# Optimization experiments

Measured on AMD Instinct MI355X. Metric: run time of the kernel, lower is better.

The kernel has to match this reference:

```python
import jax, jax.numpy as jnp
import numpy as np

N, C, H, W = 16, 80, 200, 152
STRIDE = 8
PRE_NMS_THRESH = 0.2
K = 100            # pre_nms_top_n (== fpn_post_nms_top_n)
NMS_THRESH = 0.6
MIN_SIZE = 0.0


def setup_inputs() -> dict:
    key = jax.random.key(0)
    k1, k2, k3 = jax.random.split(key, 3)
    # shift logits down so only a realistic fraction passes sigmoid > 0.2
    box_cls = jax.random.normal(k1, (N, C, H, W), jnp.float32) - 2.0
    box_regression = jax.random.uniform(k2, (N, 4, H, W), jnp.float32) * 64.0
    centerness = jax.random.normal(k3, (N, 1, H, W), jnp.float32)
    ys, xs = jnp.meshgrid(jnp.arange(H), jnp.arange(W), indexing='ij')
    locations = jnp.stack([xs * STRIDE + STRIDE // 2,
                           ys * STRIDE + STRIDE // 2], axis=-1)
    locations = locations.reshape(-1, 2).astype(jnp.float32)  # [HW, 2] (x, y)
    return {"locations": locations, "box_cls": box_cls,
            "box_regression": box_regression, "centerness": centerness,
            "size_h": H * STRIDE, "size_w": W * STRIDE}


def _iou_matrix(boxes):
    # boxes: [K, 4] xyxy -> pairwise IoU [K, K]
    area = jnp.clip(boxes[:, 2] - boxes[:, 0], 0) * jnp.clip(boxes[:, 3] - boxes[:, 1], 0)
    lt = jnp.maximum(boxes[:, None, :2], boxes[None, :, :2])
    rb = jnp.minimum(boxes[:, None, 2:], boxes[None, :, 2:])
    wh = jnp.clip(rb - lt, 0)
    inter = wh[..., 0] * wh[..., 1]
    return inter / (area[:, None] + area[None, :] - inter + 1e-9)


def _nms_keep(iou, valid):
    # boxes assumed sorted by score (desc). Sequential greedy suppression.
    k = valid.shape[0]
    ar = jnp.arange(k)
    def body(i, keep):
        suppressed = jnp.any(keep & (ar < i) & (iou[i] > NMS_THRESH))
        return keep.at[i].set(valid[i] & ~suppressed)
    return jax.lax.fori_loop(0, k, body, valid)


def reference(locations, box_cls, box_regression, centerness, size_h, size_w):
    n, c = box_cls.shape[0], box_cls.shape[1]
    # N,C,H,W -> N,HW,C ; sigmoid scores
    scores = jax.nn.sigmoid(box_cls.transpose(0, 2, 3, 1).reshape(n, -1, c))
    reg = box_regression.transpose(0, 2, 3, 1).reshape(n, -1, 4)        # [n,HW,4]
    ctr = jax.nn.sigmoid(centerness.transpose(0, 2, 3, 1).reshape(n, -1))  # [n,HW]
    cand = scores > PRE_NMS_THRESH
    comb = scores * ctr[:, :, None]
    # masked flat scores; top-K == topk(per_pre_nms_top_n) with -inf padding
    masked = jnp.where(cand, comb, -jnp.inf).reshape(n, -1)
    vals, idx = jax.lax.top_k(masked, K)          # sorted desc, [n,K]
    valid = jnp.isfinite(vals)
    loc_idx = idx // c                            # flat location index in HW
    labels = idx % c + 1
    per_reg = jnp.take_along_axis(reg, loc_idx[:, :, None], axis=1)  # [n,K,4]
    per_loc = locations[loc_idx]                                     # [n,K,2]
    x1 = per_loc[..., 0] - per_reg[..., 0]
    y1 = per_loc[..., 1] - per_reg[..., 1]
    x2 = per_loc[..., 0] + per_reg[..., 2]
    y2 = per_loc[..., 1] + per_reg[..., 3]
    wmax = jnp.float32(size_w - 1)
    hmax = jnp.float32(size_h - 1)
    x1 = jnp.clip(x1, 0, wmax); x2 = jnp.clip(x2, 0, wmax)
    y1 = jnp.clip(y1, 0, hmax); y2 = jnp.clip(y2, 0, hmax)
    boxes = jnp.stack([x1, y1, x2, y2], axis=-1)  # [n,K,4]
    valid = valid & (x2 - x1 >= MIN_SIZE) & (y2 - y1 >= MIN_SIZE)
    # scores = sqrt(cls * centerness); double-where keeps grads finite
    scores_out = jnp.where(valid, jnp.sqrt(jnp.where(valid, vals, 1.0)), 0.0)
    # multi-class NMS: offset boxes per class so classes never overlap
    off = labels.astype(boxes.dtype) * jnp.float32(max(size_h, size_w))
    boxes_off = boxes + off[..., None]
    iou = jax.vmap(_iou_matrix)(boxes_off)        # [n,K,K]
    keep = jax.vmap(_nms_keep)(iou, valid)        # [n,K] bool
    scores_final = jnp.where(keep, scores_out, 0.0)
    return boxes, scores_final, labels, keep
```

## Files before the change

### kernel.cpp

```cpp
#include <hip/hip_runtime.h>
#include <math.h>

#define NIMG 16
#define NC   80
#define HH   200
#define WW   152
#define HWSZ (HH*WW)
#define HW4  (HWSZ/4)
#define KTOP 100
#define NBINS 4096
#define CAP   16384
#define SCAP  512
#define FCAP  1024
#define CPG   16
#define CGRP  (NC/CPG)
#define CHUNKS4 30

#define CNT_OFF  0
#define TBIN_OFF 64
#define CIDX_OFF 128
#define CVAL_OFF (128 + NIMG*CAP*4)
#define ZERO_BYTES 128

__device__ __forceinline__ float sigf(float x){ return 1.f/(1.f+expf(-x)); }

__global__ void __launch_bounds__(256) k_collect(
    const float* __restrict__ cls, const float* __restrict__ cent,
    int* __restrict__ cnt, int* __restrict__ cand_idx, float* __restrict__ cand_val)
{
  __shared__ int lcnt, gbase;
  __shared__ int   lidx[SCAP];
  __shared__ float lval[SCAP];
  const int n = blockIdx.y, g = blockIdx.z;
  const int idx4 = blockIdx.x*256 + threadIdx.x;
  if (threadIdx.x == 0) lcnt = 0;
  __syncthreads();
  if (idx4 < HW4) {
    const float4 ct4 = ((const float4*)cent)[n*HW4 + idx4];
    float cs[4];
    cs[0] = sigf(ct4.x); cs[1] = sigf(ct4.y); cs[2] = sigf(ct4.z); cs[3] = sigf(ct4.w);
    const float4* cp = (const float4*)(cls + (size_t)n*NC*HWSZ + (size_t)g*CPG*HWSZ) + idx4;
    const int hw0 = idx4*4;
    #pragma unroll 4
    for (int c = 0; c < CPG; ++c) {
      float4 v = cp[(size_t)c*HW4];
      float x[4] = {v.x, v.y, v.z, v.w};
      #pragma unroll
      for (int e = 0; e < 4; ++e) {
        if (x[e] > 0.f) {
          float s = sigf(x[e]);
          float comb = s*cs[e];
          if (comb > 0.5f) {
            int gi = (hw0+e)*NC + (g*CPG + c);
            int p = atomicAdd(&lcnt, 1);
            if (p < SCAP) { lidx[p] = gi; lval[p] = comb; }
            else {
              int gg = atomicAdd(&cnt[n], 1);
              if (gg < CAP) { cand_idx[n*CAP+gg] = gi; cand_val[n*CAP+gg] = comb; }
            }
          }
        }
      }
    }
  }
  __syncthreads();
  int nc = lcnt; if (nc > SCAP) nc = SCAP;
  if (threadIdx.x == 0) gbase = atomicAdd(&cnt[n], nc);
  __syncthreads();
  for (int i = threadIdx.x; i < nc; i += 256) {
    int g2 = gbase + i;
    if (g2 < CAP) { cand_idx[n*CAP+g2] = lidx[i]; cand_val[n*CAP+g2] = lval[i]; }
  }
}

__global__ void __launch_bounds__(256) k_fallback(
    const float* __restrict__ cls, const float* __restrict__ cent,
    int* __restrict__ cnt, int* __restrict__ tbin,
    int* __restrict__ cand_idx, float* __restrict__ cand_val)
{
  const int n = blockIdx.x, tid = threadIdx.x;
  if (cnt[n] >= KTOP) { if (tid == 0) tbin[n] = 2048; return; }
  __shared__ int lh[NBINS];
  __shared__ int sT;
  for (int b = tid; b < NBINS; b += 256) lh[b] = 0;
  __syncthreads();
  for (int hw = tid; hw < HWSZ; hw += 256) {
    float cs = sigf(cent[n*HWSZ + hw]);
    const float* cp = cls + (size_t)n*NC*HWSZ + hw;
    for (int c = 0; c < NC; ++c) {
      float s = sigf(cp[(size_t)c*HWSZ]);
      if (s > 0.2f) {
        float comb = s*cs;
        int b = (int)(comb*4096.f); if (b > 4095) b = 4095;
        atomicAdd(&lh[b], 1);
      }
    }
  }
  __syncthreads();
  if (tid == 0) {
    int run = 0, T = 0;
    for (int b = NBINS-1; b >= 0; --b) { run += lh[b]; if (run >= KTOP) { T = b; break; } }
    sT = T; tbin[n] = T;
  }
  __syncthreads();
  const int T = sT;
  for (int hw = tid; hw < HWSZ; hw += 256) {
    float cs = sigf(cent[n*HWSZ + hw]);
    const float* cp = cls + (size_t)n*NC*HWSZ + hw;
    for (int c = 0; c < NC; ++c) {
      float s = sigf(cp[(size_t)c*HWSZ]);
      if (s > 0.2f) {
        float comb = s*cs;
        if (!(comb > 0.5f)) {
          int b = (int)(comb*4096.f);
          if (b >= T) {
            int g = atomicAdd(&cnt[n], 1);
            if (g < CAP) { cand_idx[n*CAP+g] = hw*NC + c; cand_val[n*CAP+g] = comb; }
          }
        }
      }
    }
  }
}

__global__ void __launch_bounds__(256) k_final(
    const float* __restrict__ cls, const float* __restrict__ cent,
    const float* __restrict__ reg, const float* __restrict__ locs,
    const int* __restrict__ tbin, const int* __restrict__ cnt,
    const int* __restrict__ cand_idx, const float* __restrict__ cand_val,
    float* __restrict__ out)
{
  const int n = blockIdx.x, tid = threadIdx.x;
  __shared__ int rh[256];
  __shared__ int sR, fcnt;
  __shared__ int    fidx[FCAP];
  __shared__ double fval[FCAP];
  __shared__ int    topidx[KTOP];
  __shared__ double topval[KTOP];
  __shared__ float bx1[KTOP], by1[KTOP], bx2[KTOP], by2[KTOP], barea[KTOP];
  __shared__ float ox1[KTOP], oy1[KTOP], ox2[KTOP], oy2[KTOP], osc[KTOP];
  __shared__ int olab[KTOP];
  __shared__ unsigned char oval[KTOP], okeep[KTOP];
  rh[tid] = 0;
  if (tid == 0) fcnt = 0;
  for (int k = tid; k < KTOP; k += 256) topidx[k] = -1;
  __syncthreads();
  const int T = tbin[n];
  const float lo = (float)T * (1.f/4096.f);
  const float scale = 256.f / (1.f - lo);
  int m = cnt[n]; if (m > CAP) m = CAP;
  for (int i = tid; i < m; i += 256) {
    float v = cand_val[n*CAP + i];
    int b = (int)(v*4096.f); if (b > 4095) b = 4095;
    if (b >= T) {
      int r = (int)((v - lo)*scale); r = r < 0 ? 0 : (r > 255 ? 255 : r);
      atomicAdd(&rh[r], 1);
    }
  }
  __syncthreads();
  if (tid == 0) {
    int run = 0, R = 0;
    for (int r = 255; r >= 0; --r) { run += rh[r]; if (run >= KTOP) { R = r; break; } }
    sR = R;
  }
  __syncthreads();
  const int R = sR;
  for (int i = tid; i < m; i += 256) {
    float v = cand_val[n*CAP + i];
    int b = (int)(v*4096.f); if (b > 4095) b = 4095;
    if (b >= T) {
      int r = (int)((v - lo)*scale); r = r < 0 ? 0 : (r > 255 ? 255 : r);
      if (r >= R) { int p = atomicAdd(&fcnt, 1); if (p < FCAP) fidx[p] = cand_idx[n*CAP + i]; }
    }
  }
  __syncthreads();
  int mf = fcnt; if (mf > FCAP) mf = FCAP;
  for (int i = tid; i < mf; i += 256) {
    int idx = fidx[i]; int loc = idx / NC; int c = idx - loc*NC;
    double s  = 1.0/(1.0 + exp(-(double)cls[(size_t)n*NC*HWSZ + (size_t)c*HWSZ + loc]));
    double ct = 1.0/(1.0 + exp(-(double)cent[n*HWSZ + loc]));
    fval[i] = s*ct;
  }
  __syncthreads();
  for (int i = tid; i < mf; i += 256) {
    double vi = fval[i]; int ii = fidx[i]; int r = 0;
    for (int j = 0; j < mf; ++j) {
      double vj = fval[j];
      r += (vj > vi) || (vj == vi && fidx[j] < ii);
    }
    if (r < KTOP) { topidx[r] = ii; topval[r] = vi; }
  }
  __syncthreads();
  if (tid < KTOP) {
    int idx = topidx[tid];
    float x1, y1, x2, y2, sc; int lab; bool vld;
    if (idx >= 0) {
      int loc = idx / NC; int c = idx - loc*NC; lab = c + 1;
      float lx = locs[2*loc], ly = locs[2*loc + 1];
      const float* rp = reg + (size_t)n*4*HWSZ;
      float dl = rp[loc], dt = rp[HWSZ + loc], dr = rp[2*HWSZ + loc], db = rp[3*HWSZ + loc];
      const float wmax = (float)(WW*8 - 1);
      const float hmax = (float)(HH*8 - 1);
      x1 = fminf(fmaxf(lx - dl, 0.f), wmax);
      x2 = fminf(fmaxf(lx + dr, 0.f), wmax);
      y1 = fminf(fmaxf(ly - dt, 0.f), hmax);
      y2 = fminf(fmaxf(ly + db, 0.f), hmax);
      vld = (x2 - x1 >= 0.f) && (y2 - y1 >= 0.f);
      sc = vld ? sqrtf((float)topval[tid]) : 0.f;
    } else { x1 = y1 = x2 = y2 = 0.f; lab = 1; vld = false; sc = 0.f; }
    ox1[tid] = x1; oy1[tid] = y1; ox2[tid] = x2; oy2[tid] = y2;
    osc[tid] = sc; olab[tid] = lab; oval[tid] = vld ? 1 : 0;
    float off = (float)lab * 1600.0f;
    float X1 = x1 + off, Y1 = y1 + off, X2 = x2 + off, Y2 = y2 + off;
    bx1[tid] = X1; by1[tid] = Y1; bx2[tid] = X2; by2[tid] = Y2;
    barea[tid] = fmaxf(X2 - X1, 0.f) * fmaxf(Y2 - Y1, 0.f);
  }
  __syncthreads();
  if (tid < 64) {
    const int lane = tid, j1 = lane + 64;
    float a_x1 = bx1[lane], a_y1 = by1[lane], a_x2 = bx2[lane], a_y2 = by2[lane], a_ar = barea[lane];
    float c_x1 = 0, c_y1 = 0, c_x2 = 0, c_y2 = 0, c_ar = 0;
    if (j1 < KTOP) { c_x1 = bx1[j1]; c_y1 = by1[j1]; c_x2 = bx2[j1]; c_y2 = by2[j1]; c_ar = barea[j1]; }
    unsigned long long k0 = 0ull, k1 = 0ull;
    for (int i = 0; i < KTOP; ++i) {
      float ix1 = bx1[i], iy1 = by1[i], ix2 = bx2[i], iy2 = by2[i], iar = barea[i];
      bool s0 = false, s1 = false;
      if (lane < i && ((k0 >> lane) & 1ull)) {
        float w = fmaxf(fminf(ix2, a_x2) - fmaxf(ix1, a_x1), 0.f);
        float h = fmaxf(fminf(iy2, a_y2) - fmaxf(iy1, a_y1), 0.f);
        float inter = w*h;
        s0 = inter / (iar + a_ar - inter + 1e-9f) > 0.6f;
      }
      if (j1 < i && ((k1 >> lane) & 1ull)) {
        float w = fmaxf(fminf(ix2, c_x2) - fmaxf(ix1, c_x1), 0.f);
        float h = fmaxf(fminf(iy2, c_y2) - fmaxf(iy1, c_y1), 0.f);
        float inter = w*h;
        s1 = inter / (iar + c_ar - inter + 1e-9f) > 0.6f;
      }
      unsigned long long b0 = __ballot(s0), b1 = __ballot(s1);
      bool keep_i = (oval[i] != 0) && ((b0 | b1) == 0ull);
      if (keep_i) { if (i < 64) k0 |= 1ull << i; else k1 |= 1ull << (i - 64); }
    }
    okeep[lane] = (unsigned char)((k0 >> lane) & 1ull);
    if (j1 < KTOP) okeep[j1] = (unsigned char)((k1 >> lane) & 1ull);
  }
  __syncthreads();
  if (tid < KTOP) {
    float* ob = out;
    float* os = out + NIMG*KTOP*4;
    float* ol = os + NIMG*KTOP;
    float* ok = ol + NIMG*KTOP;
    int base = n*KTOP + tid;
    ob[base*4 + 0] = ox1[tid]; ob[base*4 + 1] = oy1[tid];
    ob[base*4 + 2] = ox2[tid]; ob[base*4 + 3] = oy2[tid];
    bool kp = okeep[tid] != 0;
    os[base] = kp ? osc[tid] : 0.f;
    ol[base] = (float)olab[tid];
    ok[base] = kp ? 1.f : 0.f;
  }
}

extern "C" void kernel_launch(void* const* d_in, const int* in_sizes, int n_in,
                              void* d_out, int out_size, void* d_ws, size_t ws_size,
                              hipStream_t stream) {
  const float* locs = (const float*)d_in[0];
  const float* cls  = (const float*)d_in[1];
  const float* reg  = (const float*)d_in[2];
  const float* cent = (const float*)d_in[3];
  char* ws = (char*)d_ws;
  int*   cnt      = (int*)(ws + CNT_OFF);
  int*   tbin     = (int*)(ws + TBIN_OFF);
  int*   cand_idx = (int*)(ws + CIDX_OFF);
  float* cand_val = (float*)(ws + CVAL_OFF);
  float* out = (float*)d_out;

  hipMemsetAsync(d_ws, 0, ZERO_BYTES, stream);
  dim3 gridC(CHUNKS4, NIMG, CGRP);
  k_collect<<<gridC, 256, 0, stream>>>(cls, cent, cnt, cand_idx, cand_val);
  k_fallback<<<NIMG, 256, 0, stream>>>(cls, cent, cnt, tbin, cand_idx, cand_val);
  k_final<<<NIMG, 256, 0, stream>>>(cls, cent, reg, locs, tbin, cnt,
                                    cand_idx, cand_val, out);
}
```

Measured before the change: 314.8 us.

## Drop fallback kernel, fold rare path into final, use persistent collect grid

Removes the separate fallback launch and moves its histogram-threshold recovery path into the final kernel, where it runs only when the fast candidate count is outside [K, CAP]. The common path now bins candidates directly over [0.5,1] without the tbin indirection. The collect kernel becomes a grid-stride loop over tiles with a fixed grid and more unrolling. This is meant to save one kernel launch and a global round-trip. In exchange, k_final carries a larger shared-memory footprint, and the rare path is serialized per image.

```diff
diff --git a/kernel.cpp b/kernel.cpp
--- a/kernel.cpp
+++ b/kernel.cpp
@@ -15,9 +15,10 @@
 #define CPG   16
 #define CGRP  (NC/CPG)
 #define CHUNKS4 30
+#define TILES (CHUNKS4*NIMG*CGRP)
+#define GRIDX 2048
 
 #define CNT_OFF  0
-#define TBIN_OFF 64
 #define CIDX_OFF 128
 #define CVAL_OFF (128 + NIMG*CAP*4)
 #define ZERO_BYTES 128
@@ -31,108 +32,65 @@
   __shared__ int lcnt, gbase;
   __shared__ int   lidx[SCAP];
   __shared__ float lval[SCAP];
-  const int n = blockIdx.y, g = blockIdx.z;
-  const int idx4 = blockIdx.x*256 + threadIdx.x;
-  if (threadIdx.x == 0) lcnt = 0;
-  __syncthreads();
-  if (idx4 < HW4) {
-    const float4 ct4 = ((const float4*)cent)[n*HW4 + idx4];
-    float cs[4];
-    cs[0] = sigf(ct4.x); cs[1] = sigf(ct4.y); cs[2] = sigf(ct4.z); cs[3] = sigf(ct4.w);
-    const float4* cp = (const float4*)(cls + (size_t)n*NC*HWSZ + (size_t)g*CPG*HWSZ) + idx4;
-    const int hw0 = idx4*4;
-    #pragma unroll 4
-    for (int c = 0; c < CPG; ++c) {
-      float4 v = cp[(size_t)c*HW4];
-      float x[4] = {v.x, v.y, v.z, v.w};
-      #pragma unroll
-      for (int e = 0; e < 4; ++e) {
-        if (x[e] > 0.f) {
-          float s = sigf(x[e]);
-          float comb = s*cs[e];
-          if (comb > 0.5f) {
-            int gi = (hw0+e)*NC + (g*CPG + c);
-            int p = atomicAdd(&lcnt, 1);
-            if (p < SCAP) { lidx[p] = gi; lval[p] = comb; }
-            else {
-              int gg = atomicAdd(&cnt[n], 1);
-              if (gg < CAP) { cand_idx[n*CAP+gg] = gi; cand_val[n*CAP+gg] = comb; }
+  for (int tile = blockIdx.x; tile < TILES; tile += GRIDX) {
+    const int g     = tile / (CHUNKS4*NIMG);
+    const int r     = tile - g*(CHUNKS4*NIMG);
+    const int n     = r / CHUNKS4;
+    const int chunk = r - n*CHUNKS4;
+    const int idx4  = chunk*256 + threadIdx.x;
+    if (threadIdx.x == 0) lcnt = 0;
+    __syncthreads();
+    if (idx4 < HW4) {
+      const float4 ct4 = ((const float4*)cent)[n*HW4 + idx4];
+      float cs[4];
+      cs[0] = sigf(ct4.x); cs[1] = sigf(ct4.y); cs[2] = sigf(ct4.z); cs[3] = sigf(ct4.w);
+      const float4* cp = (const float4*)(cls + (size_t)n*NC*HWSZ + (size_t)g*CPG*HWSZ) + idx4;
+      const int hw0 = idx4*4;
+      #pragma unroll 8
+      for (int c = 0; c < CPG; ++c) {
+        float4 v = cp[(size_t)c*HW4];
+        float x[4] = {v.x, v.y, v.z, v.w};
+        #pragma unroll
+        for (int e = 0; e < 4; ++e) {
+          if (x[e] > 0.f) {
+            float s = sigf(x[e]);
+            float comb = s*cs[e];
+            if (comb > 0.5f) {
+              int gi = (hw0+e)*NC + (g*CPG + c);
+              int p = atomicAdd(&lcnt, 1);
+              if (p < SCAP) { lidx[p] = gi; lval[p] = comb; }
+              else {
+                int gg = atomicAdd(&cnt[n], 1);
+                if (gg < CAP) { cand_idx[n*CAP+gg] = gi; cand_val[n*CAP+gg] = comb; }
+              }
             }
           }
         }
       }
     }
-  }
-  __syncthreads();
-  int nc = lcnt; if (nc > SCAP) nc = SCAP;
-  if (threadIdx.x == 0) gbase = atomicAdd(&cnt[n], nc);
-  __syncthreads();
-  for (int i = threadIdx.x; i < nc; i += 256) {
-    int g2 = gbase + i;
-    if (g2 < CAP) { cand_idx[n*CAP+g2] = lidx[i]; cand_val[n*CAP+g2] = lval[i]; }
-  }
-}
-
-__global__ void __launch_bounds__(256) k_fallback(
-    const float* __restrict__ cls, const float* __restrict__ cent,
-    int* __restrict__ cnt, int* __restrict__ tbin,
-    int* __restrict__ cand_idx, float* __restrict__ cand_val)
-{
-  const int n = blockIdx.x, tid = threadIdx.x;
-  if (cnt[n] >= KTOP) { if (tid == 0) tbin[n] = 2048; return; }
-  __shared__ int lh[NBINS];
-  __shared__ int sT;
-  for (int b = tid; b < NBINS; b += 256) lh[b] = 0;
-  __syncthreads();
-  for (int hw = tid; hw < HWSZ; hw += 256) {
-    float cs = sigf(cent[n*HWSZ + hw]);
-    const float* cp = cls + (size_t)n*NC*HWSZ + hw;
-    for (int c = 0; c < NC; ++c) {
-      float s = sigf(cp[(size_t)c*HWSZ]);
-      if (s > 0.2f) {
-        float comb = s*cs;
-        int b = (int)(comb*4096.f); if (b > 4095) b = 4095;
-        atomicAdd(&lh[b], 1);
-      }
-    }
-  }
-  __syncthreads();
-  if (tid == 0) {
-    int run = 0, T = 0;
-    for (int b = NBINS-1; b >= 0; --b) { run += lh[b]; if (run >= KTOP) { T = b; break; } }
-    sT = T; tbin[n] = T;
-  }
-  __syncthreads();
-  const int T = sT;
-  for (int hw = tid; hw < HWSZ; hw += 256) {
-    float cs = sigf(cent[n*HWSZ + hw]);
-    const float* cp = cls + (size_t)n*NC*HWSZ + hw;
-    for (int c = 0; c < NC; ++c) {
-      float s = sigf(cp[(size_t)c*HWSZ]);
-      if (s > 0.2f) {
-        float comb = s*cs;
-        if (!(comb > 0.5f)) {
-          int b = (int)(comb*4096.f);
-          if (b >= T) {
-            int g = atomicAdd(&cnt[n], 1);
-            if (g < CAP) { cand_idx[n*CAP+g] = hw*NC + c; cand_val[n*CAP+g] = comb; }
-          }
-        }
-      }
-    }
+    __syncthreads();
+    int nc = lcnt; if (nc > SCAP) nc = SCAP;
+    if (threadIdx.x == 0) gbase = atomicAdd(&cnt[n], nc);
+    __syncthreads();
+    for (int i = threadIdx.x; i < nc; i += 256) {
+      int g2 = gbase + i;
+      if (g2 < CAP) { cand_idx[n*CAP+g2] = lidx[i]; cand_val[n*CAP+g2] = lval[i]; }
+    }
+    __syncthreads();
   }
 }
 
 __global__ void __launch_bounds__(256) k_final(
     const float* __restrict__ cls, const float* __restrict__ cent,
     const float* __restrict__ reg, const float* __restrict__ locs,
-    const int* __restrict__ tbin, const int* __restrict__ cnt,
+    const int* __restrict__ cnt,
     const int* __restrict__ cand_idx, const float* __restrict__ cand_val,
     float* __restrict__ out)
 {
   const int n = blockIdx.x, tid = threadIdx.x;
+  __shared__ int lh[NBINS];
   __shared__ int rh[256];
-  __shared__ int sR, fcnt;
+  __shared__ int sR, sT, fcnt;
   __shared__ int    fidx[FCAP];
   __shared__ double fval[FCAP];
   __shared__ int    topidx[KTOP];
@@ -141,36 +99,67 @@
   __shared__ float ox1[KTOP], oy1[KTOP], ox2[KTOP], oy2[KTOP], osc[KTOP];
   __shared__ int olab[KTOP];
   __shared__ unsigned char oval[KTOP], okeep[KTOP];
+
   rh[tid] = 0;
   if (tid == 0) fcnt = 0;
   for (int k = tid; k < KTOP; k += 256) topidx[k] = -1;
   __syncthreads();
-  const int T = tbin[n];
-  const float lo = (float)T * (1.f/4096.f);
-  const float scale = 256.f / (1.f - lo);
-  int m = cnt[n]; if (m > CAP) m = CAP;
-  for (int i = tid; i < m; i += 256) {
-    float v = cand_val[n*CAP + i];
-    int b = (int)(v*4096.f); if (b > 4095) b = 4095;
-    if (b >= T) {
-      int r = (int)((v - lo)*scale); r = r < 0 ? 0 : (r > 255 ? 255 : r);
+
+  const int m0 = cnt[n];
+  const bool bad = (m0 < KTOP) || (m0 > CAP);
+  if (!bad) {
+    for (int i = tid; i < m0; i += 256) {
+      float v = cand_val[n*CAP + i];
+      int r = (int)((v - 0.5f)*512.f); r = r < 0 ? 0 : (r > 255 ? 255 : r);
       atomicAdd(&rh[r], 1);
     }
-  }
-  __syncthreads();
-  if (tid == 0) {
-    int run = 0, R = 0;
-    for (int r = 255; r >= 0; --r) { run += rh[r]; if (run >= KTOP) { R = r; break; } }
-    sR = R;
-  }
-  __syncthreads();
-  const int R = sR;
-  for (int i = tid; i < m; i += 256) {
-    float v = cand_val[n*CAP + i];
-    int b = (int)(v*4096.f); if (b > 4095) b = 4095;
-    if (b >= T) {
-      int r = (int)((v - lo)*scale); r = r < 0 ? 0 : (r > 255 ? 255 : r);
+    __syncthreads();
+    if (tid == 0) {
+      int run = 0, R = 0;
+      for (int r = 255; r >= 0; --r) { run += rh[r]; if (run >= KTOP) { R = r; break; } }
+      sR = R;
+    }
+    __syncthreads();
+    const int R = sR;
+    for (int i = tid; i < m0; i += 256) {
+      float v = cand_val[n*CAP + i];
+      int r = (int)((v - 0.5f)*512.f); r = r < 0 ? 0 : (r > 255 ? 255 : r);
       if (r >= R) { int p = atomicAdd(&fcnt, 1); if (p < FCAP) fidx[p] = cand_idx[n*CAP + i]; }
+    }
+  } else {
+    for (int b = tid; b < NBINS; b += 256) lh[b] = 0;
+    __syncthreads();
+    for (int hw = tid; hw < HWSZ; hw += 256) {
+      float cs = sigf(cent[n*HWSZ + hw]);
+      const float* cp = cls + (size_t)n*NC*HWSZ + hw;
+      for (int c = 0; c < NC; ++c) {
+        float s = sigf(cp[(size_t)c*HWSZ]);
+        if (s > 0.2f) {
+          float comb = s*cs;
+          int b = (int)(comb*4096.f); if (b > 4095) b = 4095;
+          atomicAdd(&lh[b], 1);
+        }
+      }
+    }
+    __syncthreads();
+    if (tid == 0) {
+      int run = 0, T = 0;
+      for (int b = NBINS-1; b >= 0; --b) { run += lh[b]; if (run >= KTOP) { T = b; break; } }
+      sT = T;
+    }
+    __syncthreads();
+    const int T = sT;
+    for (int hw = tid; hw < HWSZ; hw += 256) {
+      float cs = sigf(cent[n*HWSZ + hw]);
+      const float* cp = cls + (size_t)n*NC*HWSZ + hw;
+      for (int c = 0; c < NC; ++c) {
+        float s = sigf(cp[(size_t)c*HWSZ]);
+        if (s > 0.2f) {
+          float comb = s*cs;
+          int b = (int)(comb*4096.f); if (b > 4095) b = 4095;
+          if (b >= T) { int p = atomicAdd(&fcnt, 1); if (p < FCAP) fidx[p] = hw*NC + c; }
+        }
+      }
     }
   }
   __syncthreads();
@@ -269,15 +258,12 @@
   const float* cent = (const float*)d_in[3];
   char* ws = (char*)d_ws;
   int*   cnt      = (int*)(ws + CNT_OFF);
-  int*   tbin     = (int*)(ws + TBIN_OFF);
   int*   cand_idx = (int*)(ws + CIDX_OFF);
   float* cand_val = (float*)(ws + CVAL_OFF);
   float* out = (float*)d_out;
 
   hipMemsetAsync(d_ws, 0, ZERO_BYTES, stream);
-  dim3 gridC(CHUNKS4, NIMG, CGRP);
-  k_collect<<<gridC, 256, 0, stream>>>(cls, cent, cnt, cand_idx, cand_val);
-  k_fallback<<<NIMG, 256, 0, stream>>>(cls, cent, cnt, tbin, cand_idx, cand_val);
-  k_final<<<NIMG, 256, 0, stream>>>(cls, cent, reg, locs, tbin, cnt,
+  k_collect<<<GRIDX, 256, 0, stream>>>(cls, cent, cnt, cand_idx, cand_val);
+  k_final<<<NIMG, 256, 0, stream>>>(cls, cent, reg, locs, cnt,
                                     cand_idx, cand_val, out);
 }
```

After: 311.2 us. About the same (-1.1%).
